# Performance work log

Hardware: AMD Instinct MI355X
Metric: run time of the kernel (lower is better)

Reference implementation:

```python
import jax, jax.numpy as jnp
import numpy as np

B, T, H, W = 4, 8, 14, 14
IN_DIMS = 768
OUT_DIMS = 768
HEADS = 12
HD = OUT_DIMS // HEADS  # 64
N = T * H * W + 1  # 1569 tokens incl. cls
SCALE = HD ** -0.5
EPS = 1e-5


def _ln(x, w, b):
    m = jnp.mean(x, -1, keepdims=True)
    v = jnp.mean((x - m) ** 2, -1, keepdims=True)
    return (x - m) * jax.lax.rsqrt(v + EPS) * w + b


def _pool(t, conv_w, nw, nb, Tq, Hq, Wq):
    # t: (B, heads, N, C) with leading cls token. Depthwise 3x3x3 conv, stride 1, pad 1.
    Bn, Hn, _, C = t.shape
    cls_tok, sp = t[:, :, :1], t[:, :, 1:]
    xc = sp.reshape(Bn * Hn, Tq, Hq, Wq, C).transpose(0, 4, 1, 2, 3)  # (B*h, C, T, H, W)
    xc = jax.lax.conv_general_dilated(
        xc, conv_w, (1, 1, 1), [(1, 1)] * 3,
        dimension_numbers=('NCDHW', 'OIDHW', 'NCDHW'), feature_group_count=C)
    xc = xc.reshape(Bn, Hn, C, Tq * Hq * Wq).swapaxes(2, 3)  # (B, h, L, C)
    xc = jnp.concatenate([cls_tok, xc], axis=2)
    return _ln(xc, nw, nb)


def _rel_lookup(rel, q_size, k_size):
    # stride_q == stride_kv == 1 -> q_size == k_size and rel already has 2*size-1 rows,
    # so no interpolation / ratio scaling is needed.
    coords = jnp.arange(q_size)[:, None] - jnp.arange(k_size)[None, :] + (k_size - 1)
    return rel[coords]  # (q, k, C)


def setup_inputs():
    key = jax.random.key(0)
    ks = jax.random.split(key, 12)
    w = lambda i, shape: jax.random.normal(ks[i], shape, jnp.float32) * 0.02
    return {
        'x': jax.random.normal(ks[0], (B, N, IN_DIMS), jnp.float32),
        'qkv_w': w(1, (IN_DIMS, 3 * OUT_DIMS)),
        'qkv_b': jnp.zeros((3 * OUT_DIMS,), jnp.float32),
        'proj_w': w(2, (OUT_DIMS, OUT_DIMS)),
        'proj_b': jnp.zeros((OUT_DIMS,), jnp.float32),
        'pool_q_w': w(3, (HD, 1, 3, 3, 3)),
        'pool_k_w': w(4, (HD, 1, 3, 3, 3)),
        'pool_v_w': w(5, (HD, 1, 3, 3, 3)),
        'norm_q_w': jnp.ones((HD,), jnp.float32), 'norm_q_b': jnp.zeros((HD,), jnp.float32),
        'norm_k_w': jnp.ones((HD,), jnp.float32), 'norm_k_b': jnp.zeros((HD,), jnp.float32),
        'norm_v_w': jnp.ones((HD,), jnp.float32), 'norm_v_b': jnp.zeros((HD,), jnp.float32),
        'rel_pos_t': w(6, (2 * T - 1, HD)),
        'rel_pos_h': w(7, (2 * H - 1, HD)),
        'rel_pos_w': w(8, (2 * W - 1, HD)),
        't_size': T, 'h_size': H, 'w_size': W,
    }


def reference(x, qkv_w, qkv_b, proj_w, proj_b, pool_q_w, pool_k_w, pool_v_w,
              norm_q_w, norm_q_b, norm_k_w, norm_k_b, norm_v_w, norm_v_b,
              rel_pos_t, rel_pos_h, rel_pos_w, t_size, h_size, w_size):
    Bn, Nn, _ = x.shape
    qkv = (x @ qkv_w + qkv_b).reshape(Bn, Nn, 3, HEADS, HD)
    qkv = jnp.transpose(qkv, (2, 0, 3, 1, 4))  # (3, B, heads, N, HD)
    q, k, v = qkv[0], qkv[1], qkv[2]
    q = _pool(q, pool_q_w, norm_q_w, norm_q_b, t_size, h_size, w_size)
    k = _pool(k, pool_k_w, norm_k_w, norm_k_b, t_size, h_size, w_size)
    v = _pool(v, pool_v_w, norm_v_w, norm_v_b, t_size, h_size, w_size)
    attn = jnp.einsum('bhqc,bhkc->bhqk', q * SCALE, k)
    # Decomposed spatiotemporal relative position bias on the non-cls block.
    Rt = _rel_lookup(rel_pos_t, t_size, t_size)
    Rh = _rel_lookup(rel_pos_h, h_size, h_size)
    Rw = _rel_lookup(rel_pos_w, w_size, w_size)
    r_q = q[:, :, 1:].reshape(Bn, HEADS, t_size, h_size, w_size, HD)
    rel_t = jnp.einsum('bythwc,tkc->bythwk', r_q, Rt)
    rel_h = jnp.einsum('bythwc,hkc->bythwk', r_q, Rh)
    rel_w = jnp.einsum('bythwc,wkc->bythwk', r_q, Rw)
    bias = (rel_t[..., :, None, None] + rel_h[..., None, :, None]
            + rel_w[..., None, None, :])  # (B, h, qt, qh, qw, kt, kh, kw)
    L = t_size * h_size * w_size
    attn = attn.at[:, :, 1:, 1:].add(bias.reshape(Bn, HEADS, L, L))
    attn = jax.nn.softmax(attn, axis=-1)
    out = jnp.einsum('bhqk,bhkc->bhqc', attn, v)
    out = out.at[:, :, 1:, :].add(q[:, :, 1:, :])  # residual pooling (cls excluded)
    out = out.swapaxes(1, 2).reshape(Bn, Nn, OUT_DIMS)
    return out @ proj_w + proj_b
```

## Files before the change

kernel.cpp:

```cpp
#include <hip/hip_runtime.h>
#include <cstdint>
#include <cstddef>

typedef __attribute__((ext_vector_type(8))) short short8;
typedef __attribute__((ext_vector_type(4))) short short4v;
typedef __attribute__((ext_vector_type(4))) float f32x4;
typedef unsigned short u16;

#define DI __device__ __forceinline__

constexpr int BATCH = 4;
constexpr int HEADS = 12, HD = 64;
constexpr int NTOK = 1569;
constexpr int NPAD = 1600;
constexpr int QPAD = 1664;
constexpr int DIM = 768, DIM3 = 2304;
constexpr int MROWS = BATCH * NTOK;
constexpr int MP = 6400;
constexpr int AUG = 128;
constexpr int BHN = BATCH * HEADS;
constexpr float LOG2E = 1.4426950408889634f;
constexpr float QSCALE = 0.125f * LOG2E;
constexpr float RESID = 8.0f / LOG2E;
constexpr float LN_EPS = 1e-5f;
constexpr int SLAB = NPAD * HD;

DI u16 f2bf(float x) {
  union { float f; unsigned u; } v; v.f = x;
  unsigned r = v.u + 0x7FFFu + ((v.u >> 16) & 1u);
  return (u16)(r >> 16);
}
DI float bf2f(u16 h) {
  union { unsigned u; float f; } v; v.u = ((unsigned)h) << 16;
  return v.f;
}

typedef const __attribute__((address_space(1))) unsigned int gu32;
typedef __attribute__((address_space(3))) unsigned int lu32;
DI void gld16(const void* g, void* l) {
  __builtin_amdgcn_global_load_lds((gu32*)g, (lu32*)l, 16, 0, 0);
}

DI float redsum64_u(float x) {
  int t;
  t = __builtin_amdgcn_update_dpp(__float_as_int(x), __float_as_int(x), 0x121, 0xF, 0xF, false);
  x += __int_as_float(t);
  t = __builtin_amdgcn_update_dpp(__float_as_int(x), __float_as_int(x), 0x122, 0xF, 0xF, false);
  x += __int_as_float(t);
  t = __builtin_amdgcn_update_dpp(__float_as_int(x), __float_as_int(x), 0x124, 0xF, 0xF, false);
  x += __int_as_float(t);
  t = __builtin_amdgcn_update_dpp(__float_as_int(x), __float_as_int(x), 0x128, 0xF, 0xF, false);
  x += __int_as_float(t);
  t = __builtin_amdgcn_update_dpp(__float_as_int(x), __float_as_int(x), 0x142, 0xF, 0xF, false);
  x += __int_as_float(t);
  t = __builtin_amdgcn_update_dpp(__float_as_int(x), __float_as_int(x), 0x143, 0xF, 0xF, false);
  x += __int_as_float(t);
  return __int_as_float(__builtin_amdgcn_readlane(__float_as_int(x), 63));
}

__global__ __launch_bounds__(256) void k_cast_x(const float* __restrict__ x,
                                                u16* __restrict__ xb) {
  int i = (blockIdx.x * 256 + threadIdx.x) * 4;
  if (i >= MP * DIM) return;
  int row = i / DIM;
  short4v o;
  if (row < MROWS) {
    float4 v = *(const float4*)(x + i);
    o.x = (short)f2bf(v.x); o.y = (short)f2bf(v.y);
    o.z = (short)f2bf(v.z); o.w = (short)f2bf(v.w);
  } else {
    o.x = 0; o.y = 0; o.z = 0; o.w = 0;
  }
  *(short4v*)(xb + i) = o;
}

__global__ __launch_bounds__(256) void k_prep(const float* __restrict__ pq,
                                              const float* __restrict__ pk,
                                              const float* __restrict__ pv,
                                              float* __restrict__ pwT) {
  int i = blockIdx.x * 256 + threadIdx.x;
  if (i >= 3 * 27 * 64) return;
  int tau = i / (27 * 64), r = i % (27 * 64);
  int tap = r >> 6, c = r & 63;
  const float* src = tau == 0 ? pq : tau == 1 ? pk : pv;
  pwT[i] = src[c * 27 + tap];
}

__global__ __launch_bounds__(256) void k_transpose_cast(const float* __restrict__ src,
                                                        u16* __restrict__ dst,
                                                        int K, int NC) {
  __shared__ float tile[32][33];
  const int ntiles = NC >> 5;
  const int bx = blockIdx.x % ntiles;
  const int by = blockIdx.x / ntiles;
  const int tx = threadIdx.x & 31, ty = threadIdx.x >> 5;
  const int n0 = bx * 32, k0 = by * 32;
#pragma unroll
  for (int r = 0; r < 32; r += 8)
    tile[ty + r][tx] = src[(size_t)(k0 + ty + r) * NC + n0 + tx];
  __syncthreads();
#pragma unroll
  for (int r = 0; r < 32; r += 8)
    dst[(size_t)(n0 + ty + r) * K + k0 + tx] = f2bf(tile[tx][ty + r]);
}

template <int EPI>
__global__ __launch_bounds__(256) void k_gemm(const u16* __restrict__ A,
                                              const u16* __restrict__ Bt,
                                              const float* __restrict__ bias,
                                              void* __restrict__ outv) {
  __shared__ __align__(16) u16 sA[2][128 * 64];
  __shared__ __align__(16) u16 sB[2][128 * 64];
  const int tid = threadIdx.x;
  const int w = tid >> 6, lane = tid & 63;
  const int g = lane >> 4, lr = lane & 15;
  const int brow = blockIdx.x * 128, bcol = blockIdx.y * 128;
  const int wr = w >> 1, wc = w & 1;

  const u16* agp[4];
  const u16* bgp[4];
  int lofs[4];
#pragma unroll
  for (int j = 0; j < 4; ++j) {
    int cb = (j * 4 + w) * 64;
    int chunk = cb + lane;
    int row = chunk >> 3, ch = chunk & 7;
    int gch = ch ^ (row & 7);
    agp[j] = A + (size_t)(brow + row) * DIM + gch * 8;
    bgp[j] = Bt + (size_t)(bcol + row) * DIM + gch * 8;
    lofs[j] = cb * 8;
  }
  auto stage = [&](int buf, int kt) {
#pragma unroll
    for (int j = 0; j < 4; ++j) {
      gld16(agp[j] + kt * 64, &sA[buf][lofs[j]]);
      gld16(bgp[j] + kt * 64, &sB[buf][lofs[j]]);
    }
  };

  f32x4 acc[4][4];
#pragma unroll
  for (int m = 0; m < 4; ++m)
#pragma unroll
    for (int n = 0; n < 4; ++n) {
      acc[m][n].x = 0.f; acc[m][n].y = 0.f; acc[m][n].z = 0.f; acc[m][n].w = 0.f;
    }

  stage(0, 0);
  __syncthreads();

  int cur = 0;
  for (int kt = 0; kt < 12; ++kt) {
    if (kt < 11) stage(cur ^ 1, kt + 1);

    short8 af[4][2], bfr[4][2];
#pragma unroll
    for (int m = 0; m < 4; ++m) {
      int row = wr * 64 + m * 16 + lr;
      int sw = row & 7;
#pragma unroll
      for (int ks = 0; ks < 2; ++ks)
        af[m][ks] = *(const short8*)&sA[cur][row * 64 + (((ks * 4 + g) ^ sw) * 8)];
    }
#pragma unroll
    for (int n = 0; n < 4; ++n) {
      int row = wc * 64 + n * 16 + lr;
      int sw = row & 7;
#pragma unroll
      for (int ks = 0; ks < 2; ++ks)
        bfr[n][ks] = *(const short8*)&sB[cur][row * 64 + (((ks * 4 + g) ^ sw) * 8)];
    }
    __builtin_amdgcn_s_setprio(1);
#pragma unroll
    for (int m = 0; m < 4; ++m)
#pragma unroll
      for (int n = 0; n < 4; ++n) {
        acc[m][n] = __builtin_amdgcn_mfma_f32_16x16x32_bf16(af[m][0], bfr[n][0], acc[m][n], 0, 0, 0);
        acc[m][n] = __builtin_amdgcn_mfma_f32_16x16x32_bf16(af[m][1], bfr[n][1], acc[m][n], 0, 0, 0);
      }
    __builtin_amdgcn_s_setprio(0);

    __syncthreads();
    cur ^= 1;
  }

#pragma unroll
  for (int m = 0; m < 4; ++m)
#pragma unroll
    for (int n = 0; n < 4; ++n) {
      int gj = bcol + wc * 64 + n * 16 + lr;
      float bv = bias[gj];
#pragma unroll
      for (int r = 0; r < 4; ++r) {
        int gm = brow + wr * 64 + m * 16 + g * 4 + r;
        if (gm >= MROWS) continue;
        float v = acc[m][n][r] + bv;
        if (EPI == 0) {
          int t = gj >= 1536 ? 2 : (gj >= 768 ? 1 : 0);
          int rem = gj - t * 768;
          int h = rem >> 6, c = rem & 63;
          int b = gm >= 3 * NTOK ? 3 : (gm >= 2 * NTOK ? 2 : (gm >= NTOK ? 1 : 0));
          int nt = gm - b * NTOK;
          ((u16*)outv)[(((size_t)(t * BATCH + b) * HEADS + h) * NPAD + nt) * HD + c] = f2bf(v);
        } else {
          ((float*)outv)[(size_t)gm * DIM + gj] = v;
        }
      }
    }
}

__global__ __launch_bounds__(256, 4) void k_pool(
    const u16* __restrict__ qkv,
    const float* __restrict__ pwT,
    const float* __restrict__ nw_q, const float* __restrict__ nb_q,
    const float* __restrict__ nw_k, const float* __restrict__ nb_k,
    const float* __restrict__ nw_v, const float* __restrict__ nb_v,
    u16* __restrict__ Qa, u16* __restrict__ Ka, u16* __restrict__ Vt) {
  const int wv = threadIdx.x >> 6, lane = threadIdx.x & 63;
  const int unit = blockIdx.x % 29;
  const int taubh = blockIdx.x / 29;
  const int tau = taubh / BHN, bh = taubh % BHN;
  const u16* src = qkv + (size_t)taubh * SLAB;
  const int zoff = (3 * BHN - taubh) * SLAB;
  const float* nw = tau == 0 ? nw_q : tau == 1 ? nw_k : nw_v;
  const float* nb = tau == 0 ? nb_q : tau == 1 ? nb_k : nb_v;

  if (unit == 28) {
    if (wv == 0) {
      float val = bf2f(src[lane]);
      float s = redsum64_u(val);
      float sq = redsum64_u(val * val);
      float mean = s * (1.f / 64.f);
      float var = sq * (1.f / 64.f) - mean * mean;
      float ln = (val - mean) * rsqrtf(var + LN_EPS) * nw[lane] + nb[lane];
      if (tau == 0)      { size_t base = (size_t)bh * QPAD * AUG; Qa[base + lane] = f2bf(ln * QSCALE); Qa[base + 64 + lane] = 0; }
      else if (tau == 1) { size_t base = (size_t)bh * NPAD * AUG; Ka[base + lane] = f2bf(ln); Ka[base + 64 + lane] = 0; }
      else               { Vt[((size_t)bh * HD + lane) * NPAD] = f2bf(ln); }
    } else {
      int lim = (tau == 0) ? QPAD : NPAD;
      for (int n = 1569 + (wv - 1); n < lim; n += 3) {
        if (tau == 0) {
          size_t base = ((size_t)bh * QPAD + n) * AUG;
          Qa[base + lane] = 0; Qa[base + 64 + lane] = 0;
        } else if (tau == 1) {
          size_t base = ((size_t)bh * NPAD + n) * AUG;
          Ka[base + lane] = 0; Ka[base + 64 + lane] = 0;
        } else {
          Vt[((size_t)bh * HD + lane) * NPAD + n] = 0;
        }
      }
    }
    return;
  }

  const int th = unit * 4 + wv;
  const int t = th / 14, hh = th % 14;

  float wt[27];
  {
    const float* wp = pwT + tau * 27 * 64 + lane;
#pragma unroll
    for (int j = 0; j < 27; ++j) wt[j] = wp[j * 64];
  }

  int roff[9];
#pragma unroll
  for (int dt = 0; dt < 3; ++dt)
#pragma unroll
    for (int dh = 0; dh < 3; ++dh) {
      int tt = t + dt - 1, h2 = hh + dh - 1;
      bool ok = ((unsigned)tt < 8u) && ((unsigned)h2 < 14u);
      roff[dt * 3 + dh] = (ok ? (1 + (tt * 14 + h2) * 14) * HD : zoff) + lane;
    }

  float win[9][4];
#pragma unroll
  for (int i = 0; i < 9; ++i) {
    win[i][0] = 0.f;
    win[i][1] = bf2f(src[roff[i]]);
    win[i][2] = bf2f(src[roff[i] + HD]);
    win[i][3] = bf2f(src[roff[i] + 2 * HD]);
  }

#pragma unroll
  for (int k = 0; k < 7; ++k) {
    const int c0 = 2 * k + 3, c1 = 2 * k + 4;
    float nxt0[9], nxt1[9];
#pragma unroll
    for (int i = 0; i < 9; ++i) {
      nxt0[i] = (c0 < 14) ? bf2f(src[roff[i] + c0 * HD]) : 0.f;
      nxt1[i] = (c1 < 14) ? bf2f(src[roff[i] + c1 * HD]) : 0.f;
    }

    float a0 = 0.f, a1 = 0.f, a2 = 0.f;
    float b0 = 0.f, b1 = 0.f, b2 = 0.f;
#pragma unroll
    for (int i = 0; i < 9; i += 3) {
      a0 += win[i][0] * wt[i * 3 + 0] + win[i][1] * wt[i * 3 + 1] + win[i][2] * wt[i * 3 + 2];
      a1 += win[i + 1][0] * wt[i * 3 + 3] + win[i + 1][1] * wt[i * 3 + 4] + win[i + 1][2] * wt[i * 3 + 5];
      a2 += win[i + 2][0] * wt[i * 3 + 6] + win[i + 2][1] * wt[i * 3 + 7] + win[i + 2][2] * wt[i * 3 + 8];
      b0 += win[i][1] * wt[i * 3 + 0] + win[i][2] * wt[i * 3 + 1] + win[i][3] * wt[i * 3 + 2];
      b1 += win[i + 1][1] * wt[i * 3 + 3] + win[i + 1][2] * wt[i * 3 + 4] + win[i + 1][3] * wt[i * 3 + 5];
      b2 += win[i + 2][1] * wt[i * 3 + 6] + win[i + 2][2] * wt[i * 3 + 7] + win[i + 2][3] * wt[i * 3 + 8];
    }
    float va = (a0 + a1) + a2;
    float vb = (b0 + b1) + b2;

    float sa = redsum64_u(va), sqa = redsum64_u(va * va);
    float sb = redsum64_u(vb), sqb = redsum64_u(vb * vb);
    float ma = sa * (1.f / 64.f), va_ = sqa * (1.f / 64.f) - ma * ma;
    float mb = sb * (1.f / 64.f), vb_ = sqb * (1.f / 64.f) - mb * mb;
    float lna = (va - ma) * rsqrtf(va_ + LN_EPS) * nw[lane] + nb[lane];
    float lnb = (vb - mb) * rsqrtf(vb_ + LN_EPS) * nw[lane] + nb[lane];

    const int n = 1 + (t * 14 + hh) * 14 + 2 * k;
    if (tau == 0) {
      size_t base = ((size_t)bh * QPAD + n) * AUG;
      Qa[base + lane] = f2bf(lna * QSCALE);
      Qa[base + 64 + lane] = 0;
      Qa[base + AUG + lane] = f2bf(lnb * QSCALE);
      Qa[base + AUG + 64 + lane] = 0;
    } else if (tau == 1) {
      size_t base = ((size_t)bh * NPAD + n) * AUG;
      Ka[base + lane] = f2bf(lna);
      Ka[base + AUG + lane] = f2bf(lnb);
      u16 ea = 0, eb = 0;
      if (lane == t || lane == 8 + hh) { ea = 0x3F80; eb = 0x3F80; }
      if (lane == 22 + 2 * k) ea = 0x3F80;
      if (lane == 23 + 2 * k) eb = 0x3F80;
      Ka[base + 64 + lane] = ea;
      Ka[base + AUG + 64 + lane] = eb;
    } else {
      size_t vb2 = ((size_t)bh * HD + lane) * NPAD + n;
      Vt[vb2] = f2bf(lna);
      Vt[vb2 + 1] = f2bf(lnb);
    }

#pragma unroll
    for (int i = 0; i < 9; ++i) {
      win[i][0] = win[i][2]; win[i][1] = win[i][3];
      win[i][2] = nxt0[i];   win[i][3] = nxt1[i];
    }
  }
}

__global__ __launch_bounds__(256) void k_rel(const float* __restrict__ rel_t,
                                             const float* __restrict__ rel_h,
                                             const float* __restrict__ rel_w,
                                             u16* __restrict__ Qa) {
  __shared__ __align__(16) u16 sR[80 * 72];
  const int tid = threadIdx.x, w = tid >> 6, lane = tid & 63;
  const int g = lane >> 4, lr = lane & 15;
  const int bh = blockIdx.x / 25, qt = blockIdx.x % 25;

  for (int idx = tid; idx < 80 * 64; idx += 256) {
    int j = idx >> 6, c = idx & 63;
    float v = 0.f;
    if (j < 15)      v = rel_t[j * HD + c];
    else if (j < 42) v = rel_h[(j - 15) * HD + c];
    else if (j < 69) v = rel_w[(j - 42) * HD + c];
    sR[j * 72 + c] = f2bf(v * 8.f);
  }
  __syncthreads();

  const int q0 = qt * 64 + w * 16;
  short8 aq[2];
  {
    const u16* qrow = Qa + ((size_t)bh * QPAD + q0 + lr) * AUG;
    aq[0] = *(const short8*)(qrow + g * 8);
    aq[1] = *(const short8*)(qrow + 32 + g * 8);
  }

  f32x4 acc[5];
#pragma unroll
  for (int jt = 0; jt < 5; ++jt) {
    f32x4 a; a.x = 0.f; a.y = 0.f; a.z = 0.f; a.w = 0.f;
    int row = jt * 16 + lr;
    short8 b0 = *(const short8*)&sR[row * 72 + g * 8];
    short8 b1 = *(const short8*)&sR[row * 72 + (4 + g) * 8];
    a = __builtin_amdgcn_mfma_f32_16x16x32_bf16(aq[0], b0, a, 0, 0, 0);
    a = __builtin_amdgcn_mfma_f32_16x16x32_bf16(aq[1], b1, a, 0, 0, 0);
    acc[jt] = a;
  }

#pragma unroll
  for (int jt = 0; jt < 5; ++jt) {
    int j = jt * 16 + lr;
#pragma unroll
    for (int r = 0; r < 4; ++r) {
      int gq = q0 + g * 4 + r;
      if (gq < 1 || gq >= NTOK) continue;
      int p = gq - 1;
      int t = p / 196, pr = p - t * 196;
      int hh = pr / 14, ww = pr - hh * 14;
      int it = t + 7 - j;
      int ih = hh + 28 - j;
      int iw = ww + 55 - j;
      int i = -1;
      if ((unsigned)it < 8u) i = it;
      else if ((unsigned)ih < 14u) i = 8 + ih;
      else if ((unsigned)iw < 14u) i = 22 + iw;
      if (i >= 0)
        Qa[((size_t)bh * QPAD + gq) * AUG + 64 + i] = f2bf(acc[jt][r]);
    }
  }
}

__global__ __launch_bounds__(256, 3) void k_attn(const u16* __restrict__ Qa,
                                                 const u16* __restrict__ Ka,
                                                 const u16* __restrict__ Vt,
                                                 u16* __restrict__ Opart,
                                                 float* __restrict__ lsum) {
  __shared__ __align__(16) u16 sK[64 * 128];
  __shared__ __align__(16) u16 sV[2][64 * 64];
  __shared__ __align__(16) u16 sP[4][32 * 72];
  const int tid = threadIdx.x, w = tid >> 6, lane = tid & 63;
  const int g = lane >> 4, lr = lane & 15;
  const int bid = blockIdx.x;
  const int swz = (bid & 7) * 156 + (bid >> 3);
  const int bh = swz / 26, rem2 = swz % 26;
  const int half = rem2 / 13, qt = rem2 % 13;
  const int qw = qt * 128 + w * 32;
  const int kb0 = half * 13;
  const int kbN = half ? 12 : 13;

  short8 aq[2][4];
#pragma unroll
  for (int f = 0; f < 2; ++f) {
    const u16* qrow = Qa + ((size_t)bh * QPAD + qw + f * 16 + lr) * AUG;
#pragma unroll
    for (int ks = 0; ks < 4; ++ks) aq[f][ks] = *(const short8*)(qrow + ks * 32 + g * 8);
  }

  short8 vones;
#pragma unroll
  for (int i = 0; i < 8; ++i) vones[i] = (short)0x3F80;

  const u16* kgp[4];
  u16* kld[4];
#pragma unroll
  for (int j = 0; j < 4; ++j) {
    int idx = j * 256 + tid;
    int row = idx >> 4, ch = idx & 15;
    int gch = ch ^ (row & 7);
    kgp[j] = Ka + ((size_t)bh * NPAD + kb0 * 64 + row) * AUG + gch * 8;
    kld[j] = &sK[(j * 256 + w * 64) * 8];
  }
  const u16* vgp[2];
  int vld[2];
#pragma unroll
  for (int j = 0; j < 2; ++j) {
    int idx = j * 256 + tid;
    int row = idx >> 3, ch = idx & 7;
    int gch = ch ^ (row & 7);
    vgp[j] = Vt + ((size_t)bh * HD + row) * NPAD + kb0 * 64 + gch * 8;
    vld[j] = (j * 256 + w * 64) * 8;
  }

#pragma unroll
  for (int j = 0; j < 4; ++j) { gld16(kgp[j], kld[j]); kgp[j] += 64 * AUG; }
#pragma unroll
  for (int j = 0; j < 2; ++j) { gld16(vgp[j], &sV[0][vld[j]]); vgp[j] += 64; }
  __syncthreads();

  f32x4 O[2][5];
#pragma unroll
  for (int f = 0; f < 2; ++f)
#pragma unroll
    for (int c4 = 0; c4 < 5; ++c4) { O[f][c4].x = 0.f; O[f][c4].y = 0.f; O[f][c4].z = 0.f; O[f][c4].w = 0.f; }

  int cur = 0;
  for (int it = 0; it < kbN; ++it) {
    f32x4 sacc[2][4];
    __builtin_amdgcn_s_setprio(1);
#pragma unroll
    for (int ct = 0; ct < 4; ++ct) {
      int row = ct * 16 + lr;
      int sw = row & 7;
      short8 bk[4];
#pragma unroll
      for (int ks = 0; ks < 4; ++ks)
        bk[ks] = *(const short8*)&sK[row * 128 + (((ks * 4 + g) ^ sw) << 3)];
#pragma unroll
      for (int f = 0; f < 2; ++f) {
        f32x4 a; a.x = 0.f; a.y = 0.f; a.z = 0.f; a.w = 0.f;
#pragma unroll
        for (int ks = 0; ks < 4; ++ks)
          a = __builtin_amdgcn_mfma_f32_16x16x32_bf16(bk[ks], aq[f][ks], a, 0, 0, 0);
        sacc[f][ct] = a;
      }
    }
    __builtin_amdgcn_s_setprio(0);
    __syncthreads();

    if (it + 1 < kbN) {
#pragma unroll
      for (int j = 0; j < 4; ++j) { gld16(kgp[j], kld[j]); kgp[j] += 64 * AUG; }
#pragma unroll
      for (int j = 0; j < 2; ++j) { gld16(vgp[j], &sV[cur ^ 1][vld[j]]); vgp[j] += 64; }
    }

    if (kb0 + it == 24) {
#pragma unroll
      for (int f = 0; f < 2; ++f) {
        sacc[f][2][0] = (g == 0) ? sacc[f][2][0] : -1e30f;
        sacc[f][2][1] = -1e30f; sacc[f][2][2] = -1e30f; sacc[f][2][3] = -1e30f;
        sacc[f][3][0] = -1e30f; sacc[f][3][1] = -1e30f;
        sacc[f][3][2] = -1e30f; sacc[f][3][3] = -1e30f;
      }
    }

#pragma unroll
    for (int f = 0; f < 2; ++f) {
      int ro = (f * 16 + lr) * 72;
#pragma unroll
      for (int ct = 0; ct < 4; ++ct) {
        unsigned u0 = __float_as_uint(exp2f(sacc[f][ct][0]));
        unsigned u1 = __float_as_uint(exp2f(sacc[f][ct][1]));
        unsigned u2 = __float_as_uint(exp2f(sacc[f][ct][2]));
        unsigned u3 = __float_as_uint(exp2f(sacc[f][ct][3]));
        uint2 pk;
        pk.x = __builtin_amdgcn_perm(u1, u0, 0x07060302u);
        pk.y = __builtin_amdgcn_perm(u3, u2, 0x07060302u);
        *(uint2*)&sP[w][ro + ct * 16 + g * 4] = pk;
      }
    }

    __builtin_amdgcn_s_setprio(1);
#pragma unroll
    for (int kk = 0; kk < 2; ++kk) {
      short8 ap[2];
#pragma unroll
      for (int f = 0; f < 2; ++f)
        ap[f] = *(const short8*)&sP[w][(f * 16 + lr) * 72 + kk * 32 + g * 8];
#pragma unroll
      for (int c4 = 0; c4 < 4; ++c4) {
        int row = c4 * 16 + lr;
        int sw = row & 7;
        short8 bv = *(const short8*)&sV[cur][row * 64 + (((kk * 4 + g) ^ sw) << 3)];
#pragma unroll
        for (int f = 0; f < 2; ++f)
          O[f][c4] = __builtin_amdgcn_mfma_f32_16x16x32_bf16(ap[f], bv, O[f][c4], 0, 0, 0);
      }
#pragma unroll
      for (int f = 0; f < 2; ++f)
        O[f][4] = __builtin_amdgcn_mfma_f32_16x16x32_bf16(ap[f], vones, O[f][4], 0, 0, 0);
    }
    __builtin_amdgcn_s_setprio(0);

    __syncthreads();
    cur ^= 1;
  }

  size_t pbase = (size_t)(bh * 2 + half) * QPAD;
#pragma unroll
  for (int f = 0; f < 2; ++f)
#pragma unroll
    for (int r = 0; r < 4; ++r) {
      int qg = qw + f * 16 + g * 4 + r;
      if (qg >= NTOK) continue;
      float l = O[f][4][r];
      float inv = 1.f / l;
#pragma unroll
      for (int c4 = 0; c4 < 4; ++c4)
        Opart[(pbase + qg) * 64 + c4 * 16 + lr] = f2bf(O[f][c4][r] * inv);
      if (lr == 0) lsum[pbase + qg] = l;
    }
}

__global__ __launch_bounds__(256) void k_comb(const u16* __restrict__ Opart,
                                              const float* __restrict__ lsum,
                                              const u16* __restrict__ Qa,
                                              u16* __restrict__ outA) {
  const int wv = threadIdx.x >> 6, lane = threadIdx.x & 63;
  int rid = blockIdx.x * 4 + wv;
  if (rid >= BHN * NTOK) return;
  int bh = rid / NTOK, qg = rid - bh * NTOK;
  size_t base0 = (size_t)(bh * 2) * QPAD + qg;
  size_t base1 = base0 + QPAD;
  float l0 = lsum[base0], l1 = lsum[base1];
  float inv = 1.f / (l0 + l1);
  float o0 = bf2f(Opart[base0 * 64 + lane]);
  float o1 = bf2f(Opart[base1 * 64 + lane]);
  float v = (l0 * o0 + l1 * o1) * inv;
  if (qg >= 1) v += RESID * bf2f(Qa[((size_t)bh * QPAD + qg) * AUG + lane]);
  int b = bh / HEADS, h = bh - b * HEADS;
  outA[((size_t)(b * NTOK + qg)) * DIM + h * HD + lane] = f2bf(v);
}

extern "C" void kernel_launch(void* const* d_in, const int* in_sizes, int n_in,
                              void* d_out, int out_size, void* d_ws, size_t ws_size,
                              hipStream_t stream) {
  (void)in_sizes; (void)n_in; (void)out_size; (void)ws_size;
  const float* x      = (const float*)d_in[0];
  const float* qkv_w  = (const float*)d_in[1];
  const float* qkv_b  = (const float*)d_in[2];
  const float* proj_w = (const float*)d_in[3];
  const float* proj_b = (const float*)d_in[4];
  const float* pw_q   = (const float*)d_in[5];
  const float* pw_k   = (const float*)d_in[6];
  const float* pw_v   = (const float*)d_in[7];
  const float* nw_q   = (const float*)d_in[8];
  const float* nb_q   = (const float*)d_in[9];
  const float* nw_k   = (const float*)d_in[10];
  const float* nb_k   = (const float*)d_in[11];
  const float* nw_v   = (const float*)d_in[12];
  const float* nb_v   = (const float*)d_in[13];
  const float* rel_t  = (const float*)d_in[14];
  const float* rel_h  = (const float*)d_in[15];
  const float* rel_w  = (const float*)d_in[16];
  float* out = (float*)d_out;

  char* ws = (char*)d_ws;
  size_t off = 0;
  auto alloc = [&](size_t bytes) -> void* {
    off = (off + 511) & ~(size_t)511;
    void* p = ws + off;
    off += bytes;
    return p;
  };
  u16*   xb     = (u16*)alloc((size_t)MP * DIM * 2);
  u16*   qkvwT  = (u16*)alloc((size_t)DIM3 * DIM * 2);
  u16*   projwT = (u16*)alloc((size_t)DIM * DIM * 2);
  u16*   qkvf   = (u16*)alloc((size_t)3 * BHN * SLAB * 2 + 2048);
  float* pwT    = (float*)alloc((size_t)3 * 27 * 64 * 4);
  u16*   Qa     = (u16*)alloc((size_t)BHN * QPAD * AUG * 2);
  u16*   Ka     = (u16*)alloc((size_t)BHN * NPAD * AUG * 2);
  u16*   Vt     = (u16*)alloc((size_t)BHN * HD * NPAD * 2);
  u16*   attnO  = (u16*)alloc((size_t)MP * DIM * 2);
  u16*   Opart  = (u16*)alloc((size_t)BHN * 2 * QPAD * HD * 2);
  float* lbuf   = (float*)alloc((size_t)BHN * 2 * QPAD * 4);

  hipMemsetAsync(qkvf + (size_t)3 * BHN * SLAB, 0, 2048, stream);

  k_cast_x<<<dim3(MP * DIM / 1024), dim3(256), 0, stream>>>(x, xb);
  k_prep<<<dim3((3 * 27 * 64 + 255) / 256), dim3(256), 0, stream>>>(pw_q, pw_k, pw_v, pwT);
  k_transpose_cast<<<dim3((DIM3 / 32) * (DIM / 32)), dim3(256), 0, stream>>>(qkv_w, qkvwT, DIM, DIM3);
  k_transpose_cast<<<dim3((DIM / 32) * (DIM / 32)), dim3(256), 0, stream>>>(proj_w, projwT, DIM, DIM);

  k_gemm<0><<<dim3(MP / 128, DIM3 / 128), dim3(256), 0, stream>>>(xb, qkvwT, qkv_b, qkvf);

  k_pool<<<dim3(3 * BHN * 29), dim3(256), 0, stream>>>(
      qkvf, pwT, nw_q, nb_q, nw_k, nb_k, nw_v, nb_v,
      Qa, Ka, Vt);

  k_rel<<<dim3(BHN * 25), dim3(256), 0, stream>>>(rel_t, rel_h, rel_w, Qa);

  k_attn<<<dim3(BHN * 26), dim3(256), 0, stream>>>(Qa, Ka, Vt, Opart, lbuf);

  k_comb<<<dim3((BHN * NTOK + 3) / 4), dim3(256), 0, stream>>>(Opart, lbuf, Qa, attnO);

  k_gemm<1><<<dim3(MP / 128, DIM / 128), dim3(256), 0, stream>>>(attnO, projwT, proj_b, out);
}
```

Before: 226.8 us.

## Triple-buffer QKV GEMM pipeline, swizzle attention P tile, drop setprio

Adds a dedicated QKV projection GEMM with three shared-memory buffers, prefetching two K-tiles ahead. It uses explicit vmcnt waits and a single barrier per iteration instead of double buffering with two syncs. The attention kernel's P staging tile drops its padded stride of 72 for an XOR-swizzled 64-wide layout, which cuts LDS use while avoiding bank conflicts. The s_setprio hints are also removed from the generic GEMM. Triple buffering raises LDS use per block, which may lower occupancy.

```diff
diff --git a/kernel.cpp b/kernel.cpp
--- a/kernel.cpp
+++ b/kernel.cpp
@@ -104,6 +104,106 @@
     dst[(size_t)(n0 + ty + r) * K + k0 + tx] = f2bf(tile[tx][ty + r]);
 }
 
+__global__ __launch_bounds__(256) void k_gemm0p(const u16* __restrict__ A,
+                                                const u16* __restrict__ Bt,
+                                                const float* __restrict__ bias,
+                                                u16* __restrict__ out) {
+  __shared__ __align__(16) u16 sA[3][128 * 64];
+  __shared__ __align__(16) u16 sB[3][128 * 64];
+  const int tid = threadIdx.x;
+  const int w = tid >> 6, lane = tid & 63;
+  const int g = lane >> 4, lr = lane & 15;
+  const int brow = blockIdx.x * 128, bcol = blockIdx.y * 128;
+  const int wr = w >> 1, wc = w & 1;
+
+  const u16* agp[4];
+  const u16* bgp[4];
+  int lofs[4];
+#pragma unroll
+  for (int j = 0; j < 4; ++j) {
+    int cb = (j * 4 + w) * 64;
+    int chunk = cb + lane;
+    int row = chunk >> 3, ch = chunk & 7;
+    int gch = ch ^ (row & 7);
+    agp[j] = A + (size_t)(brow + row) * DIM + gch * 8;
+    bgp[j] = Bt + (size_t)(bcol + row) * DIM + gch * 8;
+    lofs[j] = cb * 8;
+  }
+  auto stage = [&](int buf, int kt) {
+#pragma unroll
+    for (int j = 0; j < 4; ++j) {
+      gld16(agp[j] + kt * 64, &sA[buf][lofs[j]]);
+      gld16(bgp[j] + kt * 64, &sB[buf][lofs[j]]);
+    }
+  };
+
+  f32x4 acc[4][4];
+#pragma unroll
+  for (int m = 0; m < 4; ++m)
+#pragma unroll
+    for (int n = 0; n < 4; ++n) {
+      acc[m][n].x = 0.f; acc[m][n].y = 0.f; acc[m][n].z = 0.f; acc[m][n].w = 0.f;
+    }
+
+  stage(0, 0);
+  stage(1, 1);
+
+#pragma unroll
+  for (int kt = 0; kt < 12; ++kt) {
+    if (kt < 11) asm volatile("s_waitcnt vmcnt(8)" ::: "memory");
+    else         asm volatile("s_waitcnt vmcnt(0)" ::: "memory");
+    __builtin_amdgcn_s_barrier();
+
+    if (kt + 2 < 12) stage((kt + 2) % 3, kt + 2);
+
+    const int cur = kt % 3;
+    short8 af[4][2], bfr[4][2];
+#pragma unroll
+    for (int m = 0; m < 4; ++m) {
+      int row = wr * 64 + m * 16 + lr;
+      int sw = row & 7;
+#pragma unroll
+      for (int ks = 0; ks < 2; ++ks)
+        af[m][ks] = *(const short8*)&sA[cur][row * 64 + (((ks * 4 + g) ^ sw) * 8)];
+    }
+#pragma unroll
+    for (int n = 0; n < 4; ++n) {
+      int row = wc * 64 + n * 16 + lr;
+      int sw = row & 7;
+#pragma unroll
+      for (int ks = 0; ks < 2; ++ks)
+        bfr[n][ks] = *(const short8*)&sB[cur][row * 64 + (((ks * 4 + g) ^ sw) * 8)];
+    }
+#pragma unroll
+    for (int m = 0; m < 4; ++m)
+#pragma unroll
+      for (int n = 0; n < 4; ++n) {
+        acc[m][n] = __builtin_amdgcn_mfma_f32_16x16x32_bf16(af[m][0], bfr[n][0], acc[m][n], 0, 0, 0);
+        acc[m][n] = __builtin_amdgcn_mfma_f32_16x16x32_bf16(af[m][1], bfr[n][1], acc[m][n], 0, 0, 0);
+      }
+  }
+
+#pragma unroll
+  for (int m = 0; m < 4; ++m)
+#pragma unroll
+    for (int n = 0; n < 4; ++n) {
+      int gj = bcol + wc * 64 + n * 16 + lr;
+      float bv = bias[gj];
+#pragma unroll
+      for (int r = 0; r < 4; ++r) {
+        int gm = brow + wr * 64 + m * 16 + g * 4 + r;
+        if (gm >= MROWS) continue;
+        float v = acc[m][n][r] + bv;
+        int t = gj >= 1536 ? 2 : (gj >= 768 ? 1 : 0);
+        int rem = gj - t * 768;
+        int h = rem >> 6, c = rem & 63;
+        int b = gm >= 3 * NTOK ? 3 : (gm >= 2 * NTOK ? 2 : (gm >= NTOK ? 1 : 0));
+        int nt = gm - b * NTOK;
+        out[(((size_t)(t * BATCH + b) * HEADS + h) * NPAD + nt) * HD + c] = f2bf(v);
+      }
+    }
+}
+
 template <int EPI>
 __global__ __launch_bounds__(256) void k_gemm(const u16* __restrict__ A,
                                               const u16* __restrict__ Bt,
@@ -170,7 +270,6 @@
       for (int ks = 0; ks < 2; ++ks)
         bfr[n][ks] = *(const short8*)&sB[cur][row * 64 + (((ks * 4 + g) ^ sw) * 8)];
     }
-    __builtin_amdgcn_s_setprio(1);
 #pragma unroll
     for (int m = 0; m < 4; ++m)
 #pragma unroll
@@ -178,7 +277,6 @@
         acc[m][n] = __builtin_amdgcn_mfma_f32_16x16x32_bf16(af[m][0], bfr[n][0], acc[m][n], 0, 0, 0);
         acc[m][n] = __builtin_amdgcn_mfma_f32_16x16x32_bf16(af[m][1], bfr[n][1], acc[m][n], 0, 0, 0);
       }
-    __builtin_amdgcn_s_setprio(0);
 
     __syncthreads();
     cur ^= 1;
@@ -413,7 +511,7 @@
                                                  float* __restrict__ lsum) {
   __shared__ __align__(16) u16 sK[64 * 128];
   __shared__ __align__(16) u16 sV[2][64 * 64];
-  __shared__ __align__(16) u16 sP[4][32 * 72];
+  __shared__ __align__(16) u16 sP[4][32 * 64];
   const int tid = threadIdx.x, w = tid >> 6, lane = tid & 63;
   const int g = lane >> 4, lr = lane & 15;
   const int bid = blockIdx.x;
@@ -512,7 +610,8 @@
 
 #pragma unroll
     for (int f = 0; f < 2; ++f) {
-      int ro = (f * 16 + lr) * 72;
+      char* prow = (char*)sP[w] + (f * 16 + lr) * 128;
+      int sw4 = (lr & 7) << 4;
 #pragma unroll
       for (int ct = 0; ct < 4; ++ct) {
         unsigned u0 = __float_as_uint(exp2f(sacc[f][ct][0]));
@@ -522,7 +621,7 @@
         uint2 pk;
         pk.x = __builtin_amdgcn_perm(u1, u0, 0x07060302u);
         pk.y = __builtin_amdgcn_perm(u3, u2, 0x07060302u);
-        *(uint2*)&sP[w][ro + ct * 16 + g * 4] = pk;
+        *(uint2*)(prow + ((ct * 32 + g * 8) ^ sw4)) = pk;
       }
     }
 
@@ -531,8 +630,10 @@
     for (int kk = 0; kk < 2; ++kk) {
       short8 ap[2];
 #pragma unroll
-      for (int f = 0; f < 2; ++f)
-        ap[f] = *(const short8*)&sP[w][(f * 16 + lr) * 72 + kk * 32 + g * 8];
+      for (int f = 0; f < 2; ++f) {
+        const char* prow = (const char*)sP[w] + (f * 16 + lr) * 128;
+        ap[f] = *(const short8*)(prow + ((kk * 64 + g * 16) ^ ((lr & 7) << 4)));
+      }
 #pragma unroll
       for (int c4 = 0; c4 < 4; ++c4) {
         int row = c4 * 16 + lr;
@@ -638,7 +739,7 @@
   k_transpose_cast<<<dim3((DIM3 / 32) * (DIM / 32)), dim3(256), 0, stream>>>(qkv_w, qkvwT, DIM, DIM3);
   k_transpose_cast<<<dim3((DIM / 32) * (DIM / 32)), dim3(256), 0, stream>>>(proj_w, projwT, DIM, DIM);
 
-  k_gemm<0><<<dim3(MP / 128, DIM3 / 128), dim3(256), 0, stream>>>(xb, qkvwT, qkv_b, qkvf);
+  k_gemm0p<<<dim3(MP / 128, DIM3 / 128), dim3(256), 0, stream>>>(xb, qkvwT, qkv_b, qkvf);
 
   k_pool<<<dim3(3 * BHN * 29), dim3(256), 0, stream>>>(
       qkvf, pwT, nw_q, nb_q, nw_k, nb_k, nw_v, nb_v,
```

Result: slower. 262.5 us (+15.8%).
